# Optimization experiments

Hardware: AMD Instinct MI355X
Metric: run time of the kernel (lower is better)

The kernel has to match this reference:

```python
import jax, jax.numpy as jnp
import numpy as np

N = 10000      # nodes
E = 160000     # edges
D_IN = 512
D_H = 512
P_DROP = 0.2


def _glorot(key, shape):
    lim = float(np.sqrt(6.0 / (shape[0] + shape[1])))
    return jax.random.uniform(key, shape, jnp.float32, -lim, lim)


def setup_inputs() -> dict:
    key = jax.random.key(0)
    ks = jax.random.split(key, 8)
    h = jax.random.normal(ks[0], (N, D_IN), jnp.float32)
    src = jax.random.randint(ks[1], (E,), 0, N)
    dst = jax.random.randint(ks[2], (E,), 0, N)
    edge_weight = jax.random.uniform(ks[3], (E,), jnp.float32)
    W0 = _glorot(ks[4], (D_IN, D_H))
    W1 = _glorot(ks[5], (D_H, D_H))
    W2 = _glorot(ks[6], (D_H, D_H))
    b0 = jnp.zeros((D_H,), jnp.float32)
    b1 = jnp.zeros((D_H,), jnp.float32)
    b2 = jnp.zeros((D_H,), jnp.float32)
    return dict(h=h, src=src, dst=dst, edge_weight=edge_weight,
                W0=W0, b0=b0, W1=W1, b1=b1, W2=W2, b2=b2)


def _dropout(x, key):
    keep = jax.random.bernoulli(key, 1.0 - P_DROP, x.shape)
    return jnp.where(keep, x / (1.0 - P_DROP), 0.0)


def _graph_conv(x, src, dst, ew, W, b, act):
    # DGL GraphConv, norm='both', weight=True, bias=True, with edge_weight.
    ones = jnp.ones((src.shape[0],), x.dtype)
    deg_out = jnp.maximum(jax.ops.segment_sum(ones, src, num_segments=N), 1.0)
    deg_in = jnp.maximum(jax.ops.segment_sum(ones, dst, num_segments=N), 1.0)
    x = x * (deg_out ** -0.5)[:, None]          # src norm
    msg = x[src] * ew[:, None]                  # [E, D] gather + edge weight
    agg = jax.ops.segment_sum(msg, dst, num_segments=N)  # scatter-add
    out = (agg @ W) * (deg_in ** -0.5)[:, None] + b
    return act(out) if act is not None else out


def reference(h, src, dst, edge_weight, W0, b0, W1, b1, W2, b2):
    dk = jax.random.split(jax.random.key(42), 3)
    x = _dropout(h, dk[0])
    x = _graph_conv(x, src, dst, edge_weight, W0, b0, jax.nn.elu)
    x = _dropout(x, dk[1])
    x = _graph_conv(x, src, dst, edge_weight, W1, b1, jax.nn.elu)
    x = _dropout(x, dk[2])
    x = _graph_conv(x, src, dst, edge_weight, W2, b2, None)
    return x
```

## Files before the change

### kernel.cpp

```cpp
#include <hip/hip_runtime.h>
#include <stdint.h>

#define N_NODES 10000
#define N_EDGES 160000
#define D 512
#define TOT (N_NODES * D)
#define MASK_DW (TOT / 32)
#define FM 16
#define LDAF 520

#define HIST_B 625
#define MASK_B 1250
#define WCV_B  192
#define FILL_B 625
#define DROP_B 5000

typedef _Float16 h8 __attribute__((ext_vector_type(8)));
typedef float f4 __attribute__((ext_vector_type(4)));

__host__ __device__ inline uint32_t rotl32(uint32_t v, int r) {
    return (v << r) | (v >> (32 - r));
}

__host__ __device__ inline void tf2x32(uint32_t k0, uint32_t k1,
                                       uint32_t& x0, uint32_t& x1) {
    uint32_t k2 = k0 ^ k1 ^ 0x1BD11BDAu;
    x0 += k0; x1 += k1;
    x0 += x1; x1 = rotl32(x1, 13); x1 ^= x0;
    x0 += x1; x1 = rotl32(x1, 15); x1 ^= x0;
    x0 += x1; x1 = rotl32(x1, 26); x1 ^= x0;
    x0 += x1; x1 = rotl32(x1,  6); x1 ^= x0;
    x0 += k1; x1 += k2 + 1u;
    x0 += x1; x1 = rotl32(x1, 17); x1 ^= x0;
    x0 += x1; x1 = rotl32(x1, 29); x1 ^= x0;
    x0 += x1; x1 = rotl32(x1, 16); x1 ^= x0;
    x0 += x1; x1 = rotl32(x1, 24); x1 ^= x0;
    x0 += k2; x1 += k0 + 2u;
    x0 += x1; x1 = rotl32(x1, 13); x1 ^= x0;
    x0 += x1; x1 = rotl32(x1, 15); x1 ^= x0;
    x0 += x1; x1 = rotl32(x1, 26); x1 ^= x0;
    x0 += x1; x1 = rotl32(x1,  6); x1 ^= x0;
    x0 += k0; x1 += k1 + 3u;
    x0 += x1; x1 = rotl32(x1, 17); x1 ^= x0;
    x0 += x1; x1 = rotl32(x1, 29); x1 ^= x0;
    x0 += x1; x1 = rotl32(x1, 16); x1 ^= x0;
    x0 += x1; x1 = rotl32(x1, 24); x1 ^= x0;
    x0 += k1; x1 += k2 + 4u;
    x0 += x1; x1 = rotl32(x1, 13); x1 ^= x0;
    x0 += x1; x1 = rotl32(x1, 15); x1 ^= x0;
    x0 += x1; x1 = rotl32(x1, 26); x1 ^= x0;
    x0 += x1; x1 = rotl32(x1,  6); x1 ^= x0;
    x0 += k2; x1 += k0 + 5u;
}

__device__ __forceinline__ float dropout_gate(uint32_t k0, uint32_t k1, uint32_t j) {
    uint32_t c0 = 0u, c1 = j;
    tf2x32(k0, k1, c0, c1);
    uint32_t bits = c0 ^ c1;
    float u = __uint_as_float((bits >> 9) | 0x3f800000u) - 1.0f;
    return (u < 0.8f) ? 1.0f : 0.0f;
}

__global__ __launch_bounds__(256)
void setup1_kernel(const int* __restrict__ src, const int* __restrict__ dst,
                   int* __restrict__ deg_out, int* __restrict__ deg_in,
                   uint32_t* __restrict__ mask,
                   uint32_t k0a, uint32_t k1a, uint32_t k0b, uint32_t k1b,
                   const float* __restrict__ W0, const float* __restrict__ W1,
                   const float* __restrict__ W2, _Float16* __restrict__ Wt) {
    __shared__ float tile[64][65];
    int b = blockIdx.x;
    int tid = threadIdx.x;
    if (b < HIST_B) {
        int e = b * 256 + tid;
        if (e < N_EDGES) {
            atomicAdd(&deg_out[src[e]], 1);
            atomicAdd(&deg_in[dst[e]], 1);
        }
    } else if (b < HIST_B + MASK_B) {
        int t = (b - HIST_B) * 256 + tid;
        int layer = (t >= MASK_DW) ? 1 : 0;
        uint32_t k0 = layer ? k0b : k0a;
        uint32_t k1 = layer ? k1b : k1a;
        uint32_t base = (uint32_t)(layer ? t - MASK_DW : t) * 32u;
        uint32_t m = 0;
#pragma unroll
        for (int i = 0; i < 32; ++i) {
            uint32_t c0 = 0u, c1 = base + (uint32_t)i;
            tf2x32(k0, k1, c0, c1);
            uint32_t bits = c0 ^ c1;
            float u = __uint_as_float((bits >> 9) | 0x3f800000u) - 1.0f;
            m |= (u < 0.8f ? 1u : 0u) << i;
        }
        mask[t] = m;
    } else {
        int q = b - (HIST_B + MASK_B);
        int bz = q >> 6, r = q & 63;
        int by = r >> 3, bx = r & 7;
        const float* W = (bz == 0) ? W0 : (bz == 1) ? W1 : W2;
        _Float16* T = Wt + (size_t)bz * 512 * 512;
        int r0 = by * 64, c0 = bx * 64;
        int c = tid & 63, rq = tid >> 6;
#pragma unroll
        for (int i = 0; i < 16; ++i) {
            int rr = rq + i * 4;
            tile[rr][c] = W[(size_t)(r0 + rr) * 512 + c0 + c];
        }
        __syncthreads();
        int k = tid & 63, nq = tid >> 6;
#pragma unroll
        for (int i = 0; i < 16; ++i) {
            int n = nq + i * 4;
            T[(size_t)(c0 + n) * 512 + r0 + k] = (_Float16)tile[k][n];
        }
    }
}

__global__ __launch_bounds__(1024)
void scan_kernel(const int* __restrict__ deg_in, const int* __restrict__ deg_out,
                 int* __restrict__ row_ptr,
                 float* __restrict__ rn_in, float* __restrict__ rn_out) {
    __shared__ int wsum[16];
    int tid = threadIdx.x;
    int lane = tid & 63, wv = tid >> 6;
    int base = tid * 10;
    bool act = base < N_NODES;
    int d[10];
#pragma unroll
    for (int j = 0; j < 10; ++j) d[j] = 0;
    if (act) {
#pragma unroll
        for (int j = 0; j < 10; ++j) d[j] = deg_in[base + j];
    }
    int tot = 0;
#pragma unroll
    for (int j = 0; j < 10; ++j) tot += d[j];
    int s = tot;
#pragma unroll
    for (int off = 1; off < 64; off <<= 1) {
        int u = __shfl_up(s, off, 64);
        if (lane >= off) s += u;
    }
    if (lane == 63) wsum[wv] = s;
    __syncthreads();
    if (wv == 0 && lane < 16) {
        int ws = wsum[lane];
#pragma unroll
        for (int off = 1; off < 16; off <<= 1) {
            int u = __shfl_up(ws, off, 64);
            if (lane >= off) ws += u;
        }
        wsum[lane] = ws;
    }
    __syncthreads();
    if (act) {
        int run = ((wv > 0) ? wsum[wv - 1] : 0) + (s - tot);
#pragma unroll
        for (int j = 0; j < 10; ++j) {
            int i = base + j;
            row_ptr[i] = run;
            int v = d[j];
            rn_in[i]  = 1.0f / sqrtf(fmaxf((float)v, 1.0f));
            rn_out[i] = 1.0f / sqrtf(fmaxf((float)deg_out[i], 1.0f));
            run += v;
        }
    }
    if (tid == 0) row_ptr[N_NODES] = wsum[15];
}

__global__ __launch_bounds__(256)
void setup2_kernel(const int* __restrict__ src, const int* __restrict__ dst,
                   const float* __restrict__ ew, const int* __restrict__ row_ptr,
                   int* __restrict__ cursor, int2* __restrict__ csr,
                   const float* __restrict__ x, _Float16* __restrict__ y,
                   const float* __restrict__ rn_out, uint32_t k0, uint32_t k1) {
    int b = blockIdx.x;
    int tid = threadIdx.x;
    if (b < FILL_B) {
        int e = b * 256 + tid;
        if (e < N_EDGES) {
            int v = dst[e];
            int pos = atomicAdd(&cursor[v], 1);
            csr[row_ptr[v] + pos] = make_int2(src[e], __float_as_int(ew[e]));
        }
    } else {
        int t = (b - FILL_B) * 256 + tid;
        int j = t * 4;
        if (j < TOT) {
            float4 xv = *(const float4*)&x[j];
            float w = rn_out[j >> 9];
            _Float16 r[4];
            uint32_t jj = (uint32_t)j;
#pragma unroll
            for (int i = 0; i < 4; ++i) {
                float g = dropout_gate(k0, k1, jj + (uint32_t)i);
                float xi = (&xv.x)[i];
                r[i] = (_Float16)(g * (xi / 0.8f) * w);
            }
            *(ushort4*)&y[j] = *(ushort4*)r;
        }
    }
}

__global__ __launch_bounds__(256)
void layer_kernel(const _Float16* __restrict__ yin, const int* __restrict__ row_ptr,
                  const int2* __restrict__ csr, const _Float16* __restrict__ Wt,
                  const float* __restrict__ bias, const float* __restrict__ rn_in,
                  const float* __restrict__ rn_out, const uint32_t* __restrict__ mask,
                  _Float16* __restrict__ yout, float* __restrict__ fout, int mode) {
    __shared__ _Float16 As[FM * LDAF];
    int tid = threadIdx.x;
    int wv = tid >> 6, lane = tid & 63;
    int row0 = blockIdx.x * FM;

#pragma unroll 1
    for (int nn = 0; nn < 4; ++nn) {
        int ln = wv * 4 + nn;
        int node = row0 + ln;
        float acc[8] = {0, 0, 0, 0, 0, 0, 0, 0};
        int beg = row_ptr[node], end = row_ptr[node + 1];
        int k = beg;
        for (; k + 7 < end; k += 8) {
            h8 a[8];
            float w[8];
#pragma unroll
            for (int q = 0; q < 8; ++q) {
                int2 e = csr[k + q];
                a[q] = *(const h8*)&yin[(size_t)e.x * 512 + lane * 8];
                w[q] = __int_as_float(e.y);
            }
#pragma unroll
            for (int q = 0; q < 8; ++q)
#pragma unroll
                for (int i = 0; i < 8; ++i) acc[i] += w[q] * (float)a[q][i];
        }
        for (; k + 3 < end; k += 4) {
            h8 a[4];
            float w[4];
#pragma unroll
            for (int q = 0; q < 4; ++q) {
                int2 e = csr[k + q];
                a[q] = *(const h8*)&yin[(size_t)e.x * 512 + lane * 8];
                w[q] = __int_as_float(e.y);
            }
#pragma unroll
            for (int q = 0; q < 4; ++q)
#pragma unroll
                for (int i = 0; i < 8; ++i) acc[i] += w[q] * (float)a[q][i];
        }
        for (; k < end; ++k) {
            int2 e0 = csr[k];
            float w0 = __int_as_float(e0.y);
            h8 a = *(const h8*)&yin[(size_t)e0.x * 512 + lane * 8];
#pragma unroll
            for (int i = 0; i < 8; ++i) acc[i] += w0 * (float)a[i];
        }
        _Float16 r[8];
#pragma unroll
        for (int i = 0; i < 8; ++i) r[i] = (_Float16)acc[i];
        *(h8*)&As[ln * LDAF + lane * 8] = *(h8*)r;
    }
    __syncthreads();

    f4 acc[8];
#pragma unroll
    for (int i = 0; i < 8; ++i) acc[i] = (f4){0.f, 0.f, 0.f, 0.f};

    int kf = (lane >> 4) * 8;
    const _Float16* fa = &As[(lane & 15) * LDAF + kf];
    int col0 = wv * 128;
    const _Float16* gB = Wt + (size_t)(col0 + (lane & 15)) * 512 + kf;

#pragma unroll 2
    for (int kk = 0; kk < 512; kk += 32) {
        h8 af = *(const h8*)(fa + kk);
        h8 bf[8];
#pragma unroll
        for (int nt = 0; nt < 8; ++nt)
            bf[nt] = *(const h8*)(gB + (size_t)nt * 16 * 512 + kk);
#pragma unroll
        for (int nt = 0; nt < 8; ++nt)
            acc[nt] = __builtin_amdgcn_mfma_f32_16x16x32_f16(af, bf[nt],
                                                             acc[nt], 0, 0, 0);
    }

    int gr0 = row0 + (lane >> 4) * 4;
#pragma unroll
    for (int nt = 0; nt < 8; ++nt) {
        int gc = col0 + nt * 16 + (lane & 15);
        float bcol = bias[gc];
#pragma unroll
        for (int i = 0; i < 4; ++i) {
            int gr = gr0 + i;
            float v = acc[nt][i] * rn_in[gr] + bcol;
            if (mode == 0) {
                v = (v > 0.f) ? v : expm1f(v);
                uint32_t m = mask[gr * 16 + (gc >> 5)];
                float keep = (float)((m >> (gc & 31)) & 1u);
                v = keep * (v / 0.8f) * rn_out[gr];
                yout[(size_t)gr * 512 + gc] = (_Float16)v;
            } else {
                fout[(size_t)gr * 512 + gc] = v;
            }
        }
    }
}

extern "C" void kernel_launch(void* const* d_in, const int* in_sizes, int n_in,
                              void* d_out, int out_size, void* d_ws, size_t ws_size,
                              hipStream_t stream) {
    const float* h   = (const float*)d_in[0];
    const int*   src = (const int*)d_in[1];
    const int*   dst = (const int*)d_in[2];
    const float* ew  = (const float*)d_in[3];
    const float* W0  = (const float*)d_in[4];
    const float* b0  = (const float*)d_in[5];
    const float* W1  = (const float*)d_in[6];
    const float* b1  = (const float*)d_in[7];
    const float* W2  = (const float*)d_in[8];
    const float* b2  = (const float*)d_in[9];
    const float* bl[3] = {b0, b1, b2};
    float* out = (float*)d_out;

    char* ws = (char*)d_ws;
    _Float16* yA   = (_Float16*)ws; ws += (size_t)TOT * 2;
    _Float16* yB   = (_Float16*)ws; ws += (size_t)TOT * 2;
    _Float16* Wt   = (_Float16*)ws; ws += (size_t)3 * 512 * 512 * 2;
    uint32_t* mask = (uint32_t*)ws; ws += (size_t)2 * MASK_DW * 4;
    int* degi_in  = (int*)ws;  ws += N_NODES * 4;
    int* degi_out = (int*)ws;  ws += N_NODES * 4;
    int* cursor   = (int*)ws;  ws += N_NODES * 4;
    int* row_ptr  = (int*)ws;  ws += (N_NODES + 1) * 4;
    ws = (char*)(((uintptr_t)ws + 15) & ~(uintptr_t)15);
    int2* csr     = (int2*)ws; ws += (size_t)N_EDGES * 8;
    float* rn_in  = (float*)ws; ws += N_NODES * 4;
    float* rn_out = (float*)ws; ws += N_NODES * 4;

    hipMemsetAsync(degi_in, 0, 3 * N_NODES * 4, stream);

    uint32_t dk[3][2];
    for (int i = 0; i < 3; ++i) {
        uint32_t c0 = 0u, c1 = (uint32_t)i;
        tf2x32(0u, 42u, c0, c1);
        dk[i][0] = c0; dk[i][1] = c1;
    }

    setup1_kernel<<<HIST_B + MASK_B + WCV_B, 256, 0, stream>>>(
        src, dst, degi_out, degi_in, mask,
        dk[1][0], dk[1][1], dk[2][0], dk[2][1], W0, W1, W2, Wt);
    scan_kernel<<<1, 1024, 0, stream>>>(degi_in, degi_out, row_ptr, rn_in, rn_out);
    setup2_kernel<<<FILL_B + DROP_B, 256, 0, stream>>>(
        src, dst, ew, row_ptr, cursor, csr, h, yA, rn_out, dk[0][0], dk[0][1]);

    const int NBLK = N_NODES / FM;
    layer_kernel<<<NBLK, 256, 0, stream>>>(yA, row_ptr, csr, Wt, bl[0],
                                           rn_in, rn_out, mask, yB, out, 0);
    layer_kernel<<<NBLK, 256, 0, stream>>>(yB, row_ptr, csr, Wt + (size_t)512 * 512,
                                           bl[1], rn_in, rn_out, mask + MASK_DW,
                                           yA, out, 0);
    layer_kernel<<<NBLK, 256, 0, stream>>>(yA, row_ptr, csr, Wt + (size_t)2 * 512 * 512,
                                           bl[2], rn_in, rn_out, nullptr,
                                           nullptr, out, 1);
}
```

Measured before the change: 349.7 us.

## Use 32-row, 1024-thread blocks with a 2x2 MFMA tile per wave

The fused layer kernel now processes 32 nodes per block with 16 waves instead of 16 nodes with 4 waves. Each wave aggregates 2 nodes and computes a 32x32 output tile using a 2x2 set of MFMAs, so every weight fragment is reused across two row tiles and global weight traffic per output row is halved. Bounds checks are added because 313 blocks over-cover the 10000 nodes. The cost is far fewer blocks (313 vs 625) at 1024 threads each, which can lower occupancy and hurt load balance during the irregular gather phase.

```diff
diff --git a/kernel.cpp b/kernel.cpp
--- a/kernel.cpp
+++ b/kernel.cpp
@@ -6,7 +6,8 @@
 #define D 512
 #define TOT (N_NODES * D)
 #define MASK_DW (TOT / 32)
-#define FM 16
+#define FM 32
+#define NBLK 313
 #define LDAF 520
 
 #define HIST_B 625
@@ -202,7 +203,7 @@
     }
 }
 
-__global__ __launch_bounds__(256)
+__global__ __launch_bounds__(1024)
 void layer_kernel(const _Float16* __restrict__ yin, const int* __restrict__ row_ptr,
                   const int2* __restrict__ csr, const _Float16* __restrict__ Wt,
                   const float* __restrict__ bias, const float* __restrict__ rn_in,
@@ -214,46 +215,48 @@
     int row0 = blockIdx.x * FM;
 
 #pragma unroll 1
-    for (int nn = 0; nn < 4; ++nn) {
-        int ln = wv * 4 + nn;
+    for (int nn = 0; nn < 2; ++nn) {
+        int ln = wv * 2 + nn;
         int node = row0 + ln;
         float acc[8] = {0, 0, 0, 0, 0, 0, 0, 0};
-        int beg = row_ptr[node], end = row_ptr[node + 1];
-        int k = beg;
-        for (; k + 7 < end; k += 8) {
-            h8 a[8];
-            float w[8];
-#pragma unroll
-            for (int q = 0; q < 8; ++q) {
-                int2 e = csr[k + q];
-                a[q] = *(const h8*)&yin[(size_t)e.x * 512 + lane * 8];
-                w[q] = __int_as_float(e.y);
-            }
-#pragma unroll
-            for (int q = 0; q < 8; ++q)
-#pragma unroll
-                for (int i = 0; i < 8; ++i) acc[i] += w[q] * (float)a[q][i];
-        }
-        for (; k + 3 < end; k += 4) {
-            h8 a[4];
-            float w[4];
-#pragma unroll
-            for (int q = 0; q < 4; ++q) {
-                int2 e = csr[k + q];
-                a[q] = *(const h8*)&yin[(size_t)e.x * 512 + lane * 8];
-                w[q] = __int_as_float(e.y);
-            }
-#pragma unroll
-            for (int q = 0; q < 4; ++q)
-#pragma unroll
-                for (int i = 0; i < 8; ++i) acc[i] += w[q] * (float)a[q][i];
-        }
-        for (; k < end; ++k) {
-            int2 e0 = csr[k];
-            float w0 = __int_as_float(e0.y);
-            h8 a = *(const h8*)&yin[(size_t)e0.x * 512 + lane * 8];
-#pragma unroll
-            for (int i = 0; i < 8; ++i) acc[i] += w0 * (float)a[i];
+        if (node < N_NODES) {
+            int beg = row_ptr[node], end = row_ptr[node + 1];
+            int k = beg;
+            for (; k + 7 < end; k += 8) {
+                h8 a[8];
+                float w[8];
+#pragma unroll
+                for (int q = 0; q < 8; ++q) {
+                    int2 e = csr[k + q];
+                    a[q] = *(const h8*)&yin[(size_t)e.x * 512 + lane * 8];
+                    w[q] = __int_as_float(e.y);
+                }
+#pragma unroll
+                for (int q = 0; q < 8; ++q)
+#pragma unroll
+                    for (int i = 0; i < 8; ++i) acc[i] += w[q] * (float)a[q][i];
+            }
+            for (; k + 3 < end; k += 4) {
+                h8 a[4];
+                float w[4];
+#pragma unroll
+                for (int q = 0; q < 4; ++q) {
+                    int2 e = csr[k + q];
+                    a[q] = *(const h8*)&yin[(size_t)e.x * 512 + lane * 8];
+                    w[q] = __int_as_float(e.y);
+                }
+#pragma unroll
+                for (int q = 0; q < 4; ++q)
+#pragma unroll
+                    for (int i = 0; i < 8; ++i) acc[i] += w[q] * (float)a[q][i];
+            }
+            for (; k < end; ++k) {
+                int2 e0 = csr[k];
+                float w0 = __int_as_float(e0.y);
+                h8 a = *(const h8*)&yin[(size_t)e0.x * 512 + lane * 8];
+#pragma unroll
+                for (int i = 0; i < 8; ++i) acc[i] += w0 * (float)a[i];
+            }
         }
         _Float16 r[8];
 #pragma unroll
@@ -262,45 +265,51 @@
     }
     __syncthreads();
 
-    f4 acc[8];
-#pragma unroll
-    for (int i = 0; i < 8; ++i) acc[i] = (f4){0.f, 0.f, 0.f, 0.f};
+    f4 acc[2][2];
+#pragma unroll
+    for (int i = 0; i < 2; ++i)
+#pragma unroll
+        for (int j = 0; j < 2; ++j) acc[i][j] = (f4){0.f, 0.f, 0.f, 0.f};
 
     int kf = (lane >> 4) * 8;
     const _Float16* fa = &As[(lane & 15) * LDAF + kf];
-    int col0 = wv * 128;
-    const _Float16* gB = Wt + (size_t)(col0 + (lane & 15)) * 512 + kf;
-
-#pragma unroll 2
+    int col0 = wv * 32;
+    const _Float16* gB0 = Wt + (size_t)(col0 + (lane & 15)) * 512 + kf;
+    const _Float16* gB1 = gB0 + (size_t)16 * 512;
+
+#pragma unroll 4
     for (int kk = 0; kk < 512; kk += 32) {
-        h8 af = *(const h8*)(fa + kk);
-        h8 bf[8];
-#pragma unroll
-        for (int nt = 0; nt < 8; ++nt)
-            bf[nt] = *(const h8*)(gB + (size_t)nt * 16 * 512 + kk);
-#pragma unroll
-        for (int nt = 0; nt < 8; ++nt)
-            acc[nt] = __builtin_amdgcn_mfma_f32_16x16x32_f16(af, bf[nt],
-                                                             acc[nt], 0, 0, 0);
-    }
-
-    int gr0 = row0 + (lane >> 4) * 4;
-#pragma unroll
-    for (int nt = 0; nt < 8; ++nt) {
-        int gc = col0 + nt * 16 + (lane & 15);
-        float bcol = bias[gc];
-#pragma unroll
-        for (int i = 0; i < 4; ++i) {
-            int gr = gr0 + i;
-            float v = acc[nt][i] * rn_in[gr] + bcol;
-            if (mode == 0) {
-                v = (v > 0.f) ? v : expm1f(v);
-                uint32_t m = mask[gr * 16 + (gc >> 5)];
-                float keep = (float)((m >> (gc & 31)) & 1u);
-                v = keep * (v / 0.8f) * rn_out[gr];
-                yout[(size_t)gr * 512 + gc] = (_Float16)v;
-            } else {
-                fout[(size_t)gr * 512 + gc] = v;
+        h8 af0 = *(const h8*)(fa + kk);
+        h8 af1 = *(const h8*)(fa + 16 * LDAF + kk);
+        h8 bf0 = *(const h8*)(gB0 + kk);
+        h8 bf1 = *(const h8*)(gB1 + kk);
+        acc[0][0] = __builtin_amdgcn_mfma_f32_16x16x32_f16(af0, bf0, acc[0][0], 0, 0, 0);
+        acc[0][1] = __builtin_amdgcn_mfma_f32_16x16x32_f16(af0, bf1, acc[0][1], 0, 0, 0);
+        acc[1][0] = __builtin_amdgcn_mfma_f32_16x16x32_f16(af1, bf0, acc[1][0], 0, 0, 0);
+        acc[1][1] = __builtin_amdgcn_mfma_f32_16x16x32_f16(af1, bf1, acc[1][1], 0, 0, 0);
+    }
+
+#pragma unroll
+    for (int mt = 0; mt < 2; ++mt) {
+#pragma unroll
+        for (int nt = 0; nt < 2; ++nt) {
+            int gr0 = row0 + mt * 16 + (lane >> 4) * 4;
+            int gc = col0 + nt * 16 + (lane & 15);
+            float bcol = bias[gc];
+#pragma unroll
+            for (int i = 0; i < 4; ++i) {
+                int gr = gr0 + i;
+                if (gr >= N_NODES) continue;
+                float v = acc[mt][nt][i] * rn_in[gr] + bcol;
+                if (mode == 0) {
+                    v = (v > 0.f) ? v : expm1f(v);
+                    uint32_t m = mask[gr * 16 + (gc >> 5)];
+                    float keep = (float)((m >> (gc & 31)) & 1u);
+                    v = keep * (v / 0.8f) * rn_out[gr];
+                    yout[(size_t)gr * 512 + gc] = (_Float16)v;
+                } else {
+                    fout[(size_t)gr * 512 + gc] = v;
+                }
             }
         }
     }
@@ -352,13 +361,12 @@
     setup2_kernel<<<FILL_B + DROP_B, 256, 0, stream>>>(
         src, dst, ew, row_ptr, cursor, csr, h, yA, rn_out, dk[0][0], dk[0][1]);
 
-    const int NBLK = N_NODES / FM;
-    layer_kernel<<<NBLK, 256, 0, stream>>>(yA, row_ptr, csr, Wt, bl[0],
-                                           rn_in, rn_out, mask, yB, out, 0);
-    layer_kernel<<<NBLK, 256, 0, stream>>>(yB, row_ptr, csr, Wt + (size_t)512 * 512,
-                                           bl[1], rn_in, rn_out, mask + MASK_DW,
-                                           yA, out, 0);
-    layer_kernel<<<NBLK, 256, 0, stream>>>(yA, row_ptr, csr, Wt + (size_t)2 * 512 * 512,
-                                           bl[2], rn_in, rn_out, nullptr,
-                                           nullptr, out, 1);
-}
+    layer_kernel<<<NBLK, 1024, 0, stream>>>(yA, row_ptr, csr, Wt, bl[0],
+                                            rn_in, rn_out, mask, yB, out, 0);
+    layer_kernel<<<NBLK, 1024, 0, stream>>>(yB, row_ptr, csr, Wt + (size_t)512 * 512,
+                                            bl[1], rn_in, rn_out, mask + MASK_DW,
+                                            yA, out, 0);
+    layer_kernel<<<NBLK, 1024, 0, stream>>>(yA, row_ptr, csr, Wt + (size_t)2 * 512 * 512,
+                                            bl[2], rn_in, rn_out, nullptr,
+                                            nullptr, out, 1);
+}
```

After: 332.8 us. -4.8%, faster.
